# Performance work log

Hardware: AMD Instinct MI355X
Metric: run time of the kernel (lower is better)

Reference implementation:

```python
import jax, jax.numpy as jnp
import numpy as np

N, K, C, OUT = 50000, 16, 128, 128
PAD_FRAC = 0.1  # fraction of neighbor slots masked with -1


def setup_inputs() -> dict:
    key = jax.random.key(0)
    k1, k2, k3, k4, k5 = jax.random.split(key, 5)
    x = jax.random.normal(k1, (N, C), dtype=jnp.float32)
    edge_index = jax.random.randint(k2, (N, K), 0, N)
    drop = jax.random.uniform(k3, (N, K)) < PAD_FRAC
    drop = drop.at[:, 0].set(False)  # keep >=1 valid neighbor per node
    edge_index = jnp.where(drop, -1, edge_index)
    W = jax.random.normal(k4, (2 * C, OUT), dtype=jnp.float32) / np.sqrt(2.0 * C)
    b = jax.random.normal(k5, (OUT,), dtype=jnp.float32) * 0.01
    return {"x": x, "edge_index": edge_index, "W": W, "b": b}


def reference(x, edge_index, W, b):
    # Pad node table with a zero row; index -1 wraps to it (matches torch's
    # node_feature_padded[edge_index] with explicit -1 -> zeros semantics).
    padded = jnp.concatenate([x, jnp.zeros((1, x.shape[1]), x.dtype)], axis=0)
    neigh = padded[edge_index]                      # [N, K, C]
    xr = x[:, None, :]                              # [N, 1, C]
    h = jnp.concatenate(
        [jnp.broadcast_to(xr, neigh.shape), neigh - xr], axis=-1
    )                                               # [N, K, 2C]
    out = jax.nn.elu(jnp.einsum('nkc,co->nko', h, W) + b)  # [N, K, OUT]
    out = jnp.where(edge_index[..., None] != -1, out, -jnp.inf)
    return jnp.max(out, axis=1)                     # [N, OUT]
```

## Files before the change

### kernel.cpp

```cpp
#include <hip/hip_runtime.h>
#include <hip/hip_bf16.h>
#include <hip/hip_fp16.h>
#include <math.h>

#define NNODES 50000
#define KNEI 16

typedef __attribute__((ext_vector_type(8))) short bf8;
typedef __attribute__((ext_vector_type(4))) float f32x4;

static __device__ __forceinline__ unsigned short f2bf(float f) {
    __hip_bfloat16 h = __float2bfloat16(f);
    return *reinterpret_cast<unsigned short*>(&h);
}
static __device__ __forceinline__ unsigned short f2h(float f) {
    __half h = __float2half(f);
    return *reinterpret_cast<unsigned short*>(&h);
}
static __device__ __forceinline__ float2 h2f2(unsigned int u) {
    __half2 h = *reinterpret_cast<__half2*>(&u);
    return __half22float2(h);
}

__global__ __launch_bounds__(128) void prep_bt(const float* __restrict__ W,
                                               unsigned short* __restrict__ BT) {
    int c = blockIdx.x;
    int k = threadIdx.x;
    float v;
    if (c < 128) v = W[k * 128 + c] - W[(k + 128) * 128 + c];
    else         v = W[(k + 128) * 128 + (c - 128)];
    BT[c * 128 + k] = f2bf(v);
}

__global__ __launch_bounds__(256) void gemm_bf16(const float* __restrict__ x,
                                                 const unsigned short* __restrict__ BT,
                                                 const float* __restrict__ bias,
                                                 unsigned short* __restrict__ Ph,
                                                 unsigned short* __restrict__ Qh) {
    __shared__ unsigned short As[64][136];
    const int t = threadIdx.x;
    const int row0 = blockIdx.x * 64;

    #pragma unroll
    for (int i = 0; i < 8; ++i) {
        int f  = t + i * 256;
        int r  = f >> 5;
        int c4 = f & 31;
        int gr = row0 + r;
        float4 v = make_float4(0.f, 0.f, 0.f, 0.f);
        if (gr < NNODES) v = ((const float4*)x)[gr * 32 + c4];
        unsigned int u0 = (unsigned int)f2bf(v.x) | ((unsigned int)f2bf(v.y) << 16);
        unsigned int u1 = (unsigned int)f2bf(v.z) | ((unsigned int)f2bf(v.w) << 16);
        *(uint2*)&As[r][c4 * 4] = make_uint2(u0, u1);
    }
    __syncthreads();

    const int w  = t >> 6;
    const int l  = t & 63;
    const int lr = l & 15;
    const int lk = (l >> 4) * 8;
    const int ctile = blockIdx.y;

    f32x4 acc[4][2];
    #pragma unroll
    for (int m = 0; m < 4; ++m)
        #pragma unroll
        for (int n = 0; n < 2; ++n) acc[m][n] = (f32x4){0.f, 0.f, 0.f, 0.f};

    const int colL0 = w * 32 + lr;
    const unsigned short* bt0 = BT + (ctile * 128 + colL0) * 128 + lk;

    #pragma unroll
    for (int s = 0; s < 4; ++s) {
        const int kp = s * 32;
        bf8 a[4], b[2];
        #pragma unroll
        for (int m = 0; m < 4; ++m)
            a[m] = *(const bf8*)&As[m * 16 + lr][kp + lk];
        #pragma unroll
        for (int n = 0; n < 2; ++n)
            b[n] = *(const bf8*)(bt0 + n * 16 * 128 + kp);
        #pragma unroll
        for (int m = 0; m < 4; ++m)
            #pragma unroll
            for (int n = 0; n < 2; ++n)
                acc[m][n] = __builtin_amdgcn_mfma_f32_16x16x32_bf16(a[m], b[n], acc[m][n], 0, 0, 0);
    }

    const float b0v = (ctile == 0) ? bias[colL0]      : 0.f;
    const float b1v = (ctile == 0) ? bias[colL0 + 16] : 0.f;
    unsigned short* dst = (ctile == 0) ? Ph : Qh;

    __syncthreads();
    unsigned short* Ls = &As[0][0];
    #pragma unroll
    for (int m = 0; m < 4; ++m) {
        #pragma unroll
        for (int n = 0; n < 2; ++n) {
            int cl = colL0 + n * 16;
            float bb = n ? b1v : b0v;
            #pragma unroll
            for (int i = 0; i < 4; ++i) {
                int rl = m * 16 + (l >> 4) * 4 + i;
                Ls[rl * 136 + cl] = f2h(acc[m][n][i] + bb);
            }
        }
    }
    __syncthreads();

    #pragma unroll
    for (int it = 0; it < 4; ++it) {
        int cidx = t + it * 256;
        int row  = cidx >> 4;
        int seg  = cidx & 15;
        uint4 v = *(const uint4*)&Ls[row * 136 + seg * 8];
        int gr = row0 + row;
        if (gr < NNODES)
            *(uint4*)(dst + (size_t)gr * 128 + seg * 8) = v;
    }
}

__global__ __launch_bounds__(256) void gather_max(const unsigned short* __restrict__ Ph,
                                                  const unsigned short* __restrict__ Qh,
                                                  const int* __restrict__ edge,
                                                  float* __restrict__ out) {
    const int t  = threadIdx.x;
    const int n  = blockIdx.x * 16 + (t >> 4);
    const int o8 = (t & 15) * 8;

    const int4* er = (const int4*)(edge + n * KNEI);
    int4 e0 = er[0], e1 = er[1], e2 = er[2], e3 = er[3];
    int ia[16] = {e0.x, e0.y, e0.z, e0.w, e1.x, e1.y, e1.z, e1.w,
                  e2.x, e2.y, e2.z, e2.w, e3.x, e3.y, e3.z, e3.w};
    const int s0 = ia[0];
    const unsigned short* qb = Qh + o8;

    uint4 q[16];
    #pragma unroll
    for (int k = 0; k < 16; ++k) {
        int ix = ia[k] < 0 ? s0 : ia[k];
        q[k] = *(const uint4*)(qb + (size_t)ix * 128);
    }
    uint4 pv = *(const uint4*)(Ph + (size_t)n * 128 + o8);

    float2 m0 = h2f2(q[0].x), m1 = h2f2(q[0].y), m2 = h2f2(q[0].z), m3 = h2f2(q[0].w);
    #pragma unroll
    for (int k = 1; k < 16; ++k) {
        float2 a0 = h2f2(q[k].x), a1 = h2f2(q[k].y), a2 = h2f2(q[k].z), a3 = h2f2(q[k].w);
        m0.x = fmaxf(m0.x, a0.x); m0.y = fmaxf(m0.y, a0.y);
        m1.x = fmaxf(m1.x, a1.x); m1.y = fmaxf(m1.y, a1.y);
        m2.x = fmaxf(m2.x, a2.x); m2.y = fmaxf(m2.y, a2.y);
        m3.x = fmaxf(m3.x, a3.x); m3.y = fmaxf(m3.y, a3.y);
    }
    float2 p0 = h2f2(pv.x), p1 = h2f2(pv.y), p2 = h2f2(pv.z), p3 = h2f2(pv.w);

    float z[8] = {p0.x + m0.x, p0.y + m0.y, p1.x + m1.x, p1.y + m1.y,
                  p2.x + m2.x, p2.y + m2.y, p3.x + m3.x, p3.y + m3.y};
    float r[8];
    #pragma unroll
    for (int i = 0; i < 8; ++i) r[i] = z[i] > 0.f ? z[i] : expm1f(z[i]);

    float* ob = out + (size_t)n * 128 + o8;
    *(float4*)ob       = make_float4(r[0], r[1], r[2], r[3]);
    *(float4*)(ob + 4) = make_float4(r[4], r[5], r[6], r[7]);
}

extern "C" void kernel_launch(void* const* d_in, const int* in_sizes, int n_in,
                              void* d_out, int out_size, void* d_ws, size_t ws_size,
                              hipStream_t stream) {
    const float* x    = (const float*)d_in[0];
    const int*   edge = (const int*)d_in[1];
    const float* W    = (const float*)d_in[2];
    const float* bias = (const float*)d_in[3];
    float* out = (float*)d_out;

    unsigned short* Qh = (unsigned short*)d_ws;
    unsigned short* Ph = Qh + 6400000;
    unsigned short* BT = Qh + 12800000;

    prep_bt<<<256, 128, 0, stream>>>(W, BT);
    gemm_bf16<<<dim3((NNODES + 63) / 64, 2), 256, 0, stream>>>(x, BT, bias, Ph, Qh);
    gather_max<<<NNODES / 16, 256, 0, stream>>>(Ph, Qh, edge, out);
}
```

Before: 122.3 us.

## Compute both P and Q column halves per block to reuse converted x tile

The GEMM grid drops its second dimension, so each block now computes all 256 output columns (P and Q) for its 64 rows instead of one 128-column half. This avoids loading x twice from global memory and converting it to bf16 twice. In exchange, each wave holds twice the accumulators, the LDS staging buffer grows to 64x264, and there are half as many blocks, which may lower occupancy and parallelism.

```diff
diff --git a/kernel.cpp b/kernel.cpp
--- a/kernel.cpp
+++ b/kernel.cpp
@@ -37,7 +37,7 @@
                                                  const float* __restrict__ bias,
                                                  unsigned short* __restrict__ Ph,
                                                  unsigned short* __restrict__ Qh) {
-    __shared__ unsigned short As[64][136];
+    __shared__ unsigned short Ls[64 * 264];
     const int t = threadIdx.x;
     const int row0 = blockIdx.x * 64;
 
@@ -51,7 +51,7 @@
         if (gr < NNODES) v = ((const float4*)x)[gr * 32 + c4];
         unsigned int u0 = (unsigned int)f2bf(v.x) | ((unsigned int)f2bf(v.y) << 16);
         unsigned int u1 = (unsigned int)f2bf(v.z) | ((unsigned int)f2bf(v.w) << 16);
-        *(uint2*)&As[r][c4 * 4] = make_uint2(u0, u1);
+        *(uint2*)&Ls[r * 136 + c4 * 4] = make_uint2(u0, u1);
     }
     __syncthreads();
 
@@ -59,64 +59,69 @@
     const int l  = t & 63;
     const int lr = l & 15;
     const int lk = (l >> 4) * 8;
-    const int ctile = blockIdx.y;
 
-    f32x4 acc[4][2];
+    f32x4 acc[4][4];
     #pragma unroll
     for (int m = 0; m < 4; ++m)
         #pragma unroll
-        for (int n = 0; n < 2; ++n) acc[m][n] = (f32x4){0.f, 0.f, 0.f, 0.f};
+        for (int n = 0; n < 4; ++n) acc[m][n] = (f32x4){0.f, 0.f, 0.f, 0.f};
 
-    const int colL0 = w * 32 + lr;
-    const unsigned short* bt0 = BT + (ctile * 128 + colL0) * 128 + lk;
+    const int colG0 = w * 64 + lr;
+    const unsigned short* bt0 = BT + colG0 * 128 + lk;
 
     #pragma unroll
     for (int s = 0; s < 4; ++s) {
         const int kp = s * 32;
-        bf8 a[4], b[2];
+        bf8 a[4], b[4];
         #pragma unroll
         for (int m = 0; m < 4; ++m)
-            a[m] = *(const bf8*)&As[m * 16 + lr][kp + lk];
+            a[m] = *(const bf8*)&Ls[(m * 16 + lr) * 136 + kp + lk];
         #pragma unroll
-        for (int n = 0; n < 2; ++n)
+        for (int n = 0; n < 4; ++n)
             b[n] = *(const bf8*)(bt0 + n * 16 * 128 + kp);
         #pragma unroll
         for (int m = 0; m < 4; ++m)
             #pragma unroll
-            for (int n = 0; n < 2; ++n)
+            for (int n = 0; n < 4; ++n)
                 acc[m][n] = __builtin_amdgcn_mfma_f32_16x16x32_bf16(a[m], b[n], acc[m][n], 0, 0, 0);
     }
 
-    const float b0v = (ctile == 0) ? bias[colL0]      : 0.f;
-    const float b1v = (ctile == 0) ? bias[colL0 + 16] : 0.f;
-    unsigned short* dst = (ctile == 0) ? Ph : Qh;
+    float bb[4];
+    #pragma unroll
+    for (int n = 0; n < 4; ++n) {
+        int col = colG0 + n * 16;
+        bb[n] = (col < 128) ? bias[col] : 0.f;
+    }
 
     __syncthreads();
-    unsigned short* Ls = &As[0][0];
     #pragma unroll
     for (int m = 0; m < 4; ++m) {
         #pragma unroll
-        for (int n = 0; n < 2; ++n) {
-            int cl = colL0 + n * 16;
-            float bb = n ? b1v : b0v;
+        for (int n = 0; n < 4; ++n) {
+            int cg = colG0 + n * 16;
             #pragma unroll
             for (int i = 0; i < 4; ++i) {
                 int rl = m * 16 + (l >> 4) * 4 + i;
-                Ls[rl * 136 + cl] = f2h(acc[m][n][i] + bb);
+                Ls[rl * 264 + cg] = f2h(acc[m][n][i] + bb[n]);
             }
         }
     }
     __syncthreads();
 
     #pragma unroll
-    for (int it = 0; it < 4; ++it) {
+    for (int it = 0; it < 8; ++it) {
         int cidx = t + it * 256;
-        int row  = cidx >> 4;
-        int seg  = cidx & 15;
-        uint4 v = *(const uint4*)&Ls[row * 136 + seg * 8];
+        int row  = cidx >> 5;
+        int seg  = cidx & 31;
+        uint4 v = *(const uint4*)&Ls[row * 264 + seg * 8];
         int gr = row0 + row;
-        if (gr < NNODES)
-            *(uint4*)(dst + (size_t)gr * 128 + seg * 8) = v;
+        if (gr < NNODES) {
+            int col = seg * 8;
+            if (col < 128)
+                *(uint4*)(Ph + (size_t)gr * 128 + col) = v;
+            else
+                *(uint4*)(Qh + (size_t)gr * 128 + (col - 128)) = v;
+        }
     }
 }
 
@@ -179,6 +184,6 @@
     unsigned short* BT = Qh + 12800000;
 
     prep_bt<<<256, 128, 0, stream>>>(W, BT);
-    gemm_bf16<<<dim3((NNODES + 63) / 64, 2), 256, 0, stream>>>(x, BT, bias, Ph, Qh);
+    gemm_bf16<<<(NNODES + 63) / 64, 256, 0, stream>>>(x, BT, bias, Ph, Qh);
     gather_max<<<NNODES / 16, 256, 0, stream>>>(Ph, Qh, edge, out);
 }
```

After: 122.7 us. Within noise of the previous version (+0.3%).
